# Performance work log

Hardware: AMD Instinct MI355X
Metric: run time of the kernel (lower is better)

Reference implementation:

```python
import jax, jax.numpy as jnp
import numpy as np
from jax import lax

WIN = 11  # window_size


def _uniform_filter_valid(x, win):
    """Separable uniform (box) filter, VALID padding. x: [B,1,H,W].
    Equivalent to scipy uniform_filter followed by skimage's pad-cropping,
    since cropped positions only use fully-interior windows."""
    kh = jnp.full((1, 1, win, 1), 1.0 / win, dtype=x.dtype)
    kw = jnp.full((1, 1, 1, win), 1.0 / win, dtype=x.dtype)
    dn = ('NCHW', 'OIHW', 'NCHW')
    x = lax.conv_general_dilated(x, kh, (1, 1), 'VALID', dimension_numbers=dn)
    x = lax.conv_general_dilated(x, kw, (1, 1), 'VALID', dimension_numbers=dn)
    return x


def _ssim_loss(pred, target, win):
    # skimage structural_similarity with gaussian_weights=False, data_range=1.0
    data_range = 1.0
    C1 = (0.01 * data_range) ** 2
    C2 = (0.03 * data_range) ** 2
    NP = win * win
    cov_norm = NP / (NP - 1.0)  # sample covariance correction

    uf = lambda z: _uniform_filter_valid(z, win)
    ux = uf(pred)
    uy = uf(target)
    uxx = uf(pred * pred)
    uyy = uf(target * target)
    uxy = uf(pred * target)

    vx = cov_norm * (uxx - ux * ux)
    vy = cov_norm * (uyy - uy * uy)
    vxy = cov_norm * (uxy - ux * uy)

    A1 = 2.0 * ux * uy + C1
    A2 = 2.0 * vxy + C2
    B1 = ux * ux + uy * uy + C1
    B2 = vx + vy + C2
    S = (A1 * A2) / (B1 * B2)

    # mean SSIM per image, then mean over batch (identical to flat mean here)
    return 1.0 - jnp.mean(S)


def setup_inputs() -> dict:
    key = jax.random.key(0)
    k1, k2 = jax.random.split(key)
    B, C, H, W = 32, 1, 512, 512
    pred = jax.random.uniform(k1, (B, C, H, W), dtype=jnp.float32)
    target = jax.random.uniform(k2, (B, C, H, W), dtype=jnp.float32)
    return {"pred": pred, "target": target}


def reference(pred, target):
    return _ssim_loss(pred, target, WIN)
```

## Files before the change

kernel.cpp:

```cpp
#include <hip/hip_runtime.h>


#define WW 512
#define OH 502
#define BANDROWS 32
#define INV_N (1.0f / 8064128.0f)

#define DPP_ADD(x, ctrl, rmask)                                            \
    x += __int_as_float(__builtin_amdgcn_update_dpp(                       \
        0, __float_as_int(x), (ctrl), (rmask), 0xf, true))

__device__ __forceinline__ float wave_iscan(float x) {
    DPP_ADD(x, 0x111, 0xf);
    DPP_ADD(x, 0x112, 0xf);
    DPP_ADD(x, 0x114, 0xf);
    DPP_ADD(x, 0x118, 0xf);
    DPP_ADD(x, 0x142, 0xa);
    DPP_ADD(x, 0x143, 0xc);
    return x;
}

__global__ __launch_bounds__(256, 5)
void ssim_main(const float* __restrict__ Pg, const float* __restrict__ Tg,
               float* __restrict__ outp) {
    const int tid  = threadIdx.x;
    const int lane = tid & 63;
    const int wv   = tid >> 6;
    const int Wid  = blockIdx.x * 4 + wv;
    const int img   = Wid / 160;
    const int rem   = Wid - img * 160;
    const int strip = rem >> 4;
    const int band  = rem & 15;

    const int col0 = (strip == 9) ? 448 : strip * 54;
    const int y0   = band * BANDROWS;
    const int y1   = min(OH, y0 + BANDROWS);

    const int col    = col0 + lane;
    const bool active = (lane < 54) && (col >= strip * 54) && (col <= 501);

    const int base = img * (WW * WW) + col;

    float sp = 0.f, st = 0.f, sq = 0.f, sx = 0.f;
    {
        int idx = base + y0 * WW;
        #pragma unroll
        for (int r = 0; r < 10; ++r) {
            float p = Pg[idx], t = Tg[idx];
            sp += p; st += t;
            sq = fmaf(p, p, sq); sq = fmaf(t, t, sq);
            sx = fmaf(p, t, sx);
            idx += WW;
        }
    }

    int in = base + (y0 + 10) * WW;
    int io = base + y0 * WW;
    float pn = Pg[in], tn = Tg[in];
    float po = Pg[io], to = Tg[io];

    const float NP  = 121.f;
    const float cn  = 121.f / 120.f;
    const float C1n = 1e-4f * 121.f * 121.f;
    const float C2n = 9e-4f * 121.f * 121.f;

    float acc = 0.f;

    for (int y = y0; y < y1 - 1; ++y) {
        sp += pn; st += tn;
        sq = fmaf(pn, pn, sq); sq = fmaf(tn, tn, sq);
        sx = fmaf(pn, tn, sx);
        in += WW; io += WW;
        float pn2 = Pg[in], tn2 = Tg[in];
        float po2 = Pg[io], to2 = Tg[io];
        float S0 = wave_iscan(sp), S1 = wave_iscan(st);
        float S2 = wave_iscan(sq), S3 = wave_iscan(sx);
        float W0 = __shfl(S0, lane + 10) - S0 + sp;
        float W1 = __shfl(S1, lane + 10) - S1 + st;
        float W2 = __shfl(S2, lane + 10) - S2 + sq;
        float W3 = __shfl(S3, lane + 10) - S3 + sx;
        if (active) {
            float m1 = W0 * W1;
            float q1 = fmaf(W0, W0, W1 * W1);
            float A1 = fmaf(2.f, m1, C1n);
            float B1 = q1 + C1n;
            float A2 = fmaf(2.f * cn, fmaf(NP, W3, -m1), C2n);
            float B2 = fmaf(cn, fmaf(NP, W2, -q1), C2n);
            acc = fmaf(A1 * A2, __builtin_amdgcn_rcpf(B1 * B2), acc);
        }
        sp -= po; st -= to;
        sq = fmaf(po, -po, sq); sq = fmaf(to, -to, sq);
        sx = fmaf(po, -to, sx);
        pn = pn2; tn = tn2; po = po2; to = to2;
    }
    {
        sp += pn; st += tn;
        sq = fmaf(pn, pn, sq); sq = fmaf(tn, tn, sq);
        sx = fmaf(pn, tn, sx);
        float S0 = wave_iscan(sp), S1 = wave_iscan(st);
        float S2 = wave_iscan(sq), S3 = wave_iscan(sx);
        float W0 = __shfl(S0, lane + 10) - S0 + sp;
        float W1 = __shfl(S1, lane + 10) - S1 + st;
        float W2 = __shfl(S2, lane + 10) - S2 + sq;
        float W3 = __shfl(S3, lane + 10) - S3 + sx;
        if (active) {
            float m1 = W0 * W1;
            float q1 = fmaf(W0, W0, W1 * W1);
            float A1 = fmaf(2.f, m1, C1n);
            float B1 = q1 + C1n;
            float A2 = fmaf(2.f * cn, fmaf(NP, W3, -m1), C2n);
            float B2 = fmaf(cn, fmaf(NP, W2, -q1), C2n);
            acc = fmaf(A1 * A2, __builtin_amdgcn_rcpf(B1 * B2), acc);
        }
    }

    #pragma unroll
    for (int off = 32; off > 0; off >>= 1) acc += __shfl_down(acc, off);
    __shared__ float wred[4];
    if (lane == 0) wred[wv] = acc;
    __syncthreads();
    if (tid == 0) {
        float s = wred[0] + wred[1] + wred[2] + wred[3];
        float contrib = -s * INV_N;
        if (blockIdx.x == 0) contrib += 1.0f;
        atomicAdd(outp, contrib);
    }
}

extern "C" void kernel_launch(void* const* d_in, const int* in_sizes, int n_in,
                              void* d_out, int out_size, void* d_ws, size_t ws_size,
                              hipStream_t stream) {
    const float* pred = (const float*)d_in[0];
    const float* targ = (const float*)d_in[1];
    float* out = (float*)d_out;

    hipMemsetAsync(out, 0, sizeof(float), stream);
    ssim_main<<<dim3(1280), dim3(256), 0, stream>>>(pred, targ, out);
}
```

Baseline: 128.9 us.

## Process two columns per lane and keep the row window in registers

```diff
diff --git a/kernel.cpp b/kernel.cpp
--- a/kernel.cpp
+++ b/kernel.cpp
@@ -3,7 +3,7 @@
 
 #define WW 512
 #define OH 502
-#define BANDROWS 32
+#define BANDR 44
 #define INV_N (1.0f / 8064128.0f)
 
 #define DPP_ADD(x, ctrl, rmask)                                            \
@@ -20,97 +20,100 @@
     return x;
 }
 
-__global__ __launch_bounds__(256, 5)
+__device__ __forceinline__ float2 hwin(float v0, float v1, int lane) {
+    float e = v0 + v1;
+    float S = wave_iscan(e);
+    float A4 = __shfl(S, lane + 4);
+    float A5 = __shfl(S, lane + 5);
+    float v5 = __shfl(v0, lane + 5);
+    float W0 = A4 - S + e + v5;
+    float W1 = A5 - S + v1;
+    return make_float2(W0, W1);
+}
+
+__device__ __forceinline__ float ssim_term(float s0, float s1, float sq, float sx) {
+    const float NP  = 121.f;
+    const float cn  = 121.f / 120.f;
+    const float C1n = 1e-4f * 121.f * 121.f;
+    const float C2n = 9e-4f * 121.f * 121.f;
+    float m1 = s0 * s1;
+    float q1 = fmaf(s0, s0, s1 * s1);
+    float A1 = fmaf(2.f, m1, C1n);
+    float B1 = q1 + C1n;
+    float A2 = fmaf(2.f * cn, fmaf(NP, sx, -m1), C2n);
+    float B2 = fmaf(cn, fmaf(NP, sq, -q1), C2n);
+    return A1 * A2 * __builtin_amdgcn_rcpf(B1 * B2);
+}
+
+__global__ __launch_bounds__(256)
 void ssim_main(const float* __restrict__ Pg, const float* __restrict__ Tg,
                float* __restrict__ outp) {
     const int tid  = threadIdx.x;
     const int lane = tid & 63;
     const int wv   = tid >> 6;
     const int Wid  = blockIdx.x * 4 + wv;
-    const int img   = Wid / 160;
-    const int rem   = Wid - img * 160;
-    const int strip = rem >> 4;
-    const int band  = rem & 15;
+    const int img   = Wid / 60;
+    const int rem   = Wid - img * 60;
+    const int strip = rem / 12;
+    const int band  = rem - strip * 12;
 
-    const int col0 = (strip == 9) ? 448 : strip * 54;
-    const int y0   = band * BANDROWS;
-    const int y1   = min(OH, y0 + BANDROWS);
+    const int col0 = (strip == 4) ? 472 : strip * 118;
+    const int outw = (strip == 4) ? 30 : 118;
+    const int y0   = band * BANDR;
+    const int rows = min(BANDR, OH - y0);
 
-    const int col    = col0 + lane;
-    const bool active = (lane < 54) && (col >= strip * 54) && (col <= 501);
+    const int cload = min(col0 + 2 * lane, 510);
+    const bool ok   = lane < (outw >> 1);
 
-    const int base = img * (WW * WW) + col;
+    const float* Pb = Pg + img * (WW * WW);
+    const float* Tb = Tg + img * (WW * WW);
 
-    float sp = 0.f, st = 0.f, sq = 0.f, sx = 0.f;
-    {
-        int idx = base + y0 * WW;
-        #pragma unroll
-        for (int r = 0; r < 10; ++r) {
-            float p = Pg[idx], t = Tg[idx];
-            sp += p; st += t;
-            sq = fmaf(p, p, sq); sq = fmaf(t, t, sq);
-            sx = fmaf(p, t, sx);
-            idx += WW;
-        }
+    float2 prr[11], trr[11];
+    float sp0 = 0.f, sp1 = 0.f, st0 = 0.f, st1 = 0.f;
+    float sq0 = 0.f, sq1 = 0.f, sx0 = 0.f, sx1 = 0.f;
+
+    #pragma unroll
+    for (int r = 0; r < 10; ++r) {
+        float2 p = *(const float2*)(Pb + (y0 + r) * WW + cload);
+        float2 t = *(const float2*)(Tb + (y0 + r) * WW + cload);
+        prr[r] = p; trr[r] = t;
+        sp0 += p.x; sp1 += p.y; st0 += t.x; st1 += t.y;
+        sq0 = fmaf(p.x, p.x, sq0); sq0 = fmaf(t.x, t.x, sq0);
+        sq1 = fmaf(p.y, p.y, sq1); sq1 = fmaf(t.y, t.y, sq1);
+        sx0 = fmaf(p.x, t.x, sx0); sx1 = fmaf(p.y, t.y, sx1);
     }
-
-    int in = base + (y0 + 10) * WW;
-    int io = base + y0 * WW;
-    float pn = Pg[in], tn = Tg[in];
-    float po = Pg[io], to = Tg[io];
-
-    const float NP  = 121.f;
-    const float cn  = 121.f / 120.f;
-    const float C1n = 1e-4f * 121.f * 121.f;
-    const float C2n = 9e-4f * 121.f * 121.f;
+    float2 Pn = *(const float2*)(Pb + (y0 + 10) * WW + cload);
+    float2 Tn = *(const float2*)(Tb + (y0 + 10) * WW + cload);
 
     float acc = 0.f;
 
-    for (int y = y0; y < y1 - 1; ++y) {
-        sp += pn; st += tn;
-        sq = fmaf(pn, pn, sq); sq = fmaf(tn, tn, sq);
-        sx = fmaf(pn, tn, sx);
-        in += WW; io += WW;
-        float pn2 = Pg[in], tn2 = Tg[in];
-        float po2 = Pg[io], to2 = Tg[io];
-        float S0 = wave_iscan(sp), S1 = wave_iscan(st);
-        float S2 = wave_iscan(sq), S3 = wave_iscan(sx);
-        float W0 = __shfl(S0, lane + 10) - S0 + sp;
-        float W1 = __shfl(S1, lane + 10) - S1 + st;
-        float W2 = __shfl(S2, lane + 10) - S2 + sq;
-        float W3 = __shfl(S3, lane + 10) - S3 + sx;
-        if (active) {
-            float m1 = W0 * W1;
-            float q1 = fmaf(W0, W0, W1 * W1);
-            float A1 = fmaf(2.f, m1, C1n);
-            float B1 = q1 + C1n;
-            float A2 = fmaf(2.f * cn, fmaf(NP, W3, -m1), C2n);
-            float B2 = fmaf(cn, fmaf(NP, W2, -q1), C2n);
-            acc = fmaf(A1 * A2, __builtin_amdgcn_rcpf(B1 * B2), acc);
-        }
-        sp -= po; st -= to;
-        sq = fmaf(po, -po, sq); sq = fmaf(to, -to, sq);
-        sx = fmaf(po, -to, sx);
-        pn = pn2; tn = tn2; po = po2; to = to2;
-    }
-    {
-        sp += pn; st += tn;
-        sq = fmaf(pn, pn, sq); sq = fmaf(tn, tn, sq);
-        sx = fmaf(pn, tn, sx);
-        float S0 = wave_iscan(sp), S1 = wave_iscan(st);
-        float S2 = wave_iscan(sq), S3 = wave_iscan(sx);
-        float W0 = __shfl(S0, lane + 10) - S0 + sp;
-        float W1 = __shfl(S1, lane + 10) - S1 + st;
-        float W2 = __shfl(S2, lane + 10) - S2 + sq;
-        float W3 = __shfl(S3, lane + 10) - S3 + sx;
-        if (active) {
-            float m1 = W0 * W1;
-            float q1 = fmaf(W0, W0, W1 * W1);
-            float A1 = fmaf(2.f, m1, C1n);
-            float B1 = q1 + C1n;
-            float A2 = fmaf(2.f * cn, fmaf(NP, W3, -m1), C2n);
-            float B2 = fmaf(cn, fmaf(NP, W2, -q1), C2n);
-            acc = fmaf(A1 * A2, __builtin_amdgcn_rcpf(B1 * B2), acc);
+    for (int yy = 0; yy < rows; yy += 11) {
+        #pragma unroll
+        for (int j = 0; j < 11; ++j) {
+            if (yy + j < rows) {
+                const int sn = (10 + j) % 11;
+                prr[sn] = Pn; trr[sn] = Tn;
+                sp0 += Pn.x; sp1 += Pn.y; st0 += Tn.x; st1 += Tn.y;
+                sq0 = fmaf(Pn.x, Pn.x, sq0); sq0 = fmaf(Tn.x, Tn.x, sq0);
+                sq1 = fmaf(Pn.y, Pn.y, sq1); sq1 = fmaf(Tn.y, Tn.y, sq1);
+                sx0 = fmaf(Pn.x, Tn.x, sx0); sx1 = fmaf(Pn.y, Tn.y, sx1);
+                int nr = min(y0 + 11 + yy + j, 511);
+                Pn = *(const float2*)(Pb + nr * WW + cload);
+                Tn = *(const float2*)(Tb + nr * WW + cload);
+                float2 w0 = hwin(sp0, sp1, lane);
+                float2 w1 = hwin(st0, st1, lane);
+                float2 w2 = hwin(sq0, sq1, lane);
+                float2 w3 = hwin(sx0, sx1, lane);
+                if (ok) {
+                    acc += ssim_term(w0.x, w1.x, w2.x, w3.x);
+                    acc += ssim_term(w0.y, w1.y, w2.y, w3.y);
+                }
+                float2 po = prr[j], to = trr[j];
+                sp0 -= po.x; sp1 -= po.y; st0 -= to.x; st1 -= to.y;
+                sq0 = fmaf(po.x, -po.x, sq0); sq0 = fmaf(to.x, -to.x, sq0);
+                sq1 = fmaf(po.y, -po.y, sq1); sq1 = fmaf(to.y, -to.y, sq1);
+                sx0 = fmaf(po.x, -to.x, sx0); sx1 = fmaf(po.y, -to.y, sx1);
+            }
         }
     }
 
@@ -135,5 +138,5 @@
     float* out = (float*)d_out;
 
     hipMemsetAsync(out, 0, sizeof(float), stream);
-    ssim_main<<<dim3(1280), dim3(256), 0, stream>>>(pred, targ, out);
+    ssim_main<<<dim3(480), dim3(256), 0, stream>>>(pred, targ, out);
 }
```

New measurement: 108.2 us. 1.19x faster.
